# Kernel optimization log

Measured on AMD Instinct MI355X. Metric: run time of the kernel, lower is better.

Reference implementation:

```python
import jax, jax.numpy as jnp
import numpy as np

NUM_HEADS = 8      # in_channels // num_head_channels = 512 // 64
NUM_GROUPS = 32    # GroupNorm groups
EPS = 1e-5


def setup_inputs() -> dict:
    key = jax.random.key(0)
    ks = jax.random.split(key, 6)
    C = 512
    x = jax.random.normal(ks[0], (8, C, 32, 32), dtype=jnp.float32)
    gn_w = jax.random.normal(ks[1], (C,), dtype=jnp.float32) * 0.1 + 1.0
    gn_b = jax.random.normal(ks[2], (C,), dtype=jnp.float32) * 0.1
    qkv_w = jax.random.normal(ks[3], (3 * C, C), dtype=jnp.float32) / np.sqrt(C)
    qkv_b = jnp.zeros((3 * C,), dtype=jnp.float32)
    # NOTE: original zero-initializes to_out; we use small random weights so the
    # attention path contributes to the output (math is identical).
    out_w = jax.random.normal(ks[4], (C, C), dtype=jnp.float32) * 0.02
    out_b = jax.random.normal(ks[5], (C,), dtype=jnp.float32) * 0.02
    return {"x": x, "gn_w": gn_w, "gn_b": gn_b, "qkv_w": qkv_w,
            "qkv_b": qkv_b, "out_w": out_w, "out_b": out_b}


def _group_norm(net, gn_w, gn_b):
    b, c, t = net.shape
    g = net.reshape(b, NUM_GROUPS, c // NUM_GROUPS, t)
    mu = jnp.mean(g, axis=(2, 3), keepdims=True)
    var = jnp.var(g, axis=(2, 3), keepdims=True)
    n = ((g - mu) * jax.lax.rsqrt(var + EPS)).reshape(b, c, t)
    return n * gn_w[None, :, None] + gn_b[None, :, None]


def reference(x, gn_w, gn_b, qkv_w, qkv_b, out_w, out_b):
    b, c, h, w = x.shape
    area = h * w
    inp = x.reshape(b, c, area)                      # [b, c, t]
    n = _group_norm(inp, gn_w, gn_b)
    # 1x1 conv1d == channel GEMM
    qkv = jnp.einsum('oc,bct->bot', qkv_w, n) + qkv_b[None, :, None]  # [b, 3c, t]
    hd = c // NUM_HEADS
    # split_qkv_after_heads: view(b*H, 3*hd, area) then split along channel
    qkv = qkv.reshape(b * NUM_HEADS, 3 * hd, area)
    q, k, v = qkv[:, :hd], qkv[:, hd:2 * hd], qkv[:, 2 * hd:]
    scale = 1.0 / np.sqrt(np.sqrt(hd))               # sqrt-sqrt per-tensor scale
    attn = jnp.einsum('bct,bcs->bts', q * scale, k * scale)  # [bH, t, s]
    prob = jax.nn.softmax(attn, axis=-1)
    net = jnp.einsum('bts,bcs->bct', prob, v).reshape(b, c, area)
    out = jnp.einsum('oc,bct->bot', out_w, net) + out_b[None, :, None]
    return (inp + out).reshape(b, c, h, w)
```

## Files before the change

### kernel.cpp

```cpp
#include <hip/hip_runtime.h>
#include <hip/hip_bf16.h>

typedef __bf16 bf16_t;
typedef __bf16 bf16x8 __attribute__((ext_vector_type(8)));
typedef __bf16 bf16x4 __attribute__((ext_vector_type(4)));
typedef short  s16x4  __attribute__((ext_vector_type(4)));
typedef float  f32x4  __attribute__((ext_vector_type(4)));

#define B_DIM 8
#define C_DIM 512
#define T_DIM 1024
#define NH 8
#define HD 64

__device__ __forceinline__ f32x4 mfma16_bf16(bf16x4 a, bf16x4 b, f32x4 c) {
    return __builtin_amdgcn_mfma_f32_16x16x16bf16_1k(
        __builtin_bit_cast(s16x4, a), __builtin_bit_cast(s16x4, b), c, 0, 0, 0);
}

__global__ __launch_bounds__(256) void prep_w(const float* __restrict__ w1,
                                              const float* __restrict__ w2,
                                              bf16_t* __restrict__ o1,
                                              bf16_t* __restrict__ o2)
{
    int tid = blockIdx.x * 256 + threadIdx.x;
    for (int p = 0; p < 4; ++p) {
        int q = tid + p * 65536;
        const f32x4* src;
        bf16x4* dst;
        int qq;
        if (q < 196608) { src = (const f32x4*)w1; dst = (bf16x4*)o1; qq = q; }
        else            { src = (const f32x4*)w2; dst = (bf16x4*)o2; qq = q - 196608; }
        f32x4 f = src[qq];
        bf16x4 h;
        for (int j = 0; j < 4; ++j) h[j] = (bf16_t)f[j];
        dst[qq] = h;
    }
}

__global__ __launch_bounds__(256) void gn_kernel(const float* __restrict__ x,
                                                 const float* __restrict__ gw,
                                                 const float* __restrict__ gb,
                                                 bf16_t* __restrict__ n_t)
{
    __shared__ bf16_t sX[16384];
    __shared__ float sred[8];
    int tid = threadIdx.x;
    int bb  = blockIdx.x >> 5;
    int g   = blockIdx.x & 31;
    const f32x4* xg4 = reinterpret_cast<const f32x4*>(x + (size_t)(bb * C_DIM + g * 16) * T_DIM);

    float s = 0.f, sq = 0.f;
    for (int i = 0; i < 16; ++i) {
        int v = tid + i * 256;
        f32x4 f = xg4[v];
        bf16x4 h;
        for (int j = 0; j < 4; ++j) {
            s += f[j]; sq += f[j] * f[j];
            h[j] = (bf16_t)f[j];
        }
        *reinterpret_cast<bf16x4*>(sX + v * 4) = h;
    }
    for (int off = 1; off < 64; off <<= 1) {
        s  += __shfl_xor(s, off);
        sq += __shfl_xor(sq, off);
    }
    int wv = tid >> 6;
    if ((tid & 63) == 0) { sred[wv * 2] = s; sred[wv * 2 + 1] = sq; }
    __syncthreads();
    s  = sred[0] + sred[2] + sred[4] + sred[6];
    sq = sred[1] + sred[3] + sred[5] + sred[7];
    float mean = s * (1.f / 16384.f);
    float var  = sq * (1.f / 16384.f) - mean * mean;
    float rs   = rsqrtf(var + 1e-5f);

    int hf = tid & 1;
    float aa[8], bbias[8];
    for (int j = 0; j < 8; ++j) {
        int c = hf * 8 + j;
        float av = gw[g * 16 + c] * rs;
        aa[j] = av;
        bbias[j] = gb[g * 16 + c] - mean * av;
    }
    bf16_t* ob = n_t + (size_t)bb * T_DIM * C_DIM + g * 16 + hf * 8;
    for (int p = 0; p < 8; ++p) {
        int t = (tid >> 1) + p * 128;
        bf16x8 o;
        for (int j = 0; j < 8; ++j) {
            float xv = (float)sX[(hf * 8 + j) * 1024 + t];
            o[j] = (bf16_t)(xv * aa[j] + bbias[j]);
        }
        *reinterpret_cast<bf16x8*>(ob + (size_t)t * C_DIM) = o;
    }
}

__global__ __launch_bounds__(256) void qkv_gemm_kernel(
    const bf16_t* __restrict__ wqb, const float* __restrict__ bq,
    const bf16_t* __restrict__ n_t, bf16_t* __restrict__ qkv)
{
    __shared__ bf16_t sA[64 * 72];
    __shared__ bf16_t sB[128 * 72];
    int tid = threadIdx.x;
    int w = tid >> 6, lane = tid & 63, quad = lane >> 4, l15 = lane & 15;
    int bx = blockIdx.x;
    int t0 = blockIdx.y * 128;
    int bb = blockIdx.z;
    int o0 = bx * 64;
    const bf16_t* Ab = wqb + (size_t)o0 * C_DIM;
    const bf16_t* Bb = n_t + ((size_t)bb * T_DIM + t0) * C_DIM;

    f32x4 acc[2][4];
    for (int mt = 0; mt < 2; ++mt)
        for (int nt = 0; nt < 4; ++nt)
            acc[mt][nt] = f32x4{0.f, 0.f, 0.f, 0.f};
    int mw0 = (w >> 1) * 32;
    int nw0 = (w & 1) * 64;

    for (int k0 = 0; k0 < C_DIM; k0 += 64) {
        for (int i = 0; i < 2; ++i) {
            int v = tid + i * 256;
            int row = v >> 3, c8 = v & 7;
            *reinterpret_cast<bf16x8*>(sA + row * 72 + c8 * 8) =
                *reinterpret_cast<const bf16x8*>(Ab + (size_t)row * C_DIM + k0 + c8 * 8);
        }
        for (int i = 0; i < 4; ++i) {
            int v = tid + i * 256;
            int row = v >> 3, c8 = v & 7;
            *reinterpret_cast<bf16x8*>(sB + row * 72 + c8 * 8) =
                *reinterpret_cast<const bf16x8*>(Bb + (size_t)row * C_DIM + k0 + c8 * 8);
        }
        __syncthreads();
        for (int kk = 0; kk < 2; ++kk) {
            bf16x8 af[2], bfr[4];
            for (int mt = 0; mt < 2; ++mt)
                af[mt] = *reinterpret_cast<const bf16x8*>(sA + (mw0 + mt * 16 + l15) * 72 + kk * 32 + quad * 8);
            for (int nt = 0; nt < 4; ++nt)
                bfr[nt] = *reinterpret_cast<const bf16x8*>(sB + (nw0 + nt * 16 + l15) * 72 + kk * 32 + quad * 8);
            for (int mt = 0; mt < 2; ++mt)
                for (int nt = 0; nt < 4; ++nt)
                    acc[mt][nt] = __builtin_amdgcn_mfma_f32_16x16x32_bf16(af[mt], bfr[nt], acc[mt][nt], 0, 0, 0);
        }
        __syncthreads();
    }

    int h = bx / 3, type = bx % 3;
    size_t base = ((size_t)(bb * NH + h) * 3 + type) * (64 * 1024);

    if (type < 2) {
        for (int mt = 0; mt < 2; ++mt)
            for (int nt = 0; nt < 4; ++nt)
                for (int r = 0; r < 4; ++r) {
                    int mw = mw0 + mt * 16 + quad * 4 + r;
                    int tl = nw0 + nt * 16 + l15;
                    float v = acc[mt][nt][r] + bq[o0 + mw];
                    sB[tl * 72 + mw] = (bf16_t)v;
                }
        __syncthreads();
        for (int i = 0; i < 4; ++i) {
            int v = tid + i * 256;
            int tl = v >> 3, c8 = v & 7;
            bf16x8 d = *reinterpret_cast<const bf16x8*>(sB + tl * 72 + c8 * 8);
            *reinterpret_cast<bf16x8*>(qkv + base + (size_t)(t0 + tl) * 64 + c8 * 8) = d;
        }
    } else {
        for (int mt = 0; mt < 2; ++mt)
            for (int nt = 0; nt < 4; ++nt)
                for (int r = 0; r < 4; ++r) {
                    int mw = mw0 + mt * 16 + quad * 4 + r;
                    int tl = nw0 + nt * 16 + l15;
                    float v = acc[mt][nt][r] + bq[o0 + mw];
                    sB[mw * 136 + tl] = (bf16_t)v;
                }
        __syncthreads();
        for (int i = 0; i < 4; ++i) {
            int v = tid + i * 256;
            int cc = v >> 4, t8 = (v & 15) * 8;
            bf16x8 d = *reinterpret_cast<const bf16x8*>(sB + cc * 136 + t8);
            *reinterpret_cast<bf16x8*>(qkv + base + (size_t)cc * 1024 + t0 + t8) = d;
        }
    }
}

__global__ __launch_bounds__(256, 6) void attn_kernel(const bf16_t* __restrict__ qkv,
                                                      bf16_t* __restrict__ net_t)
{
    __shared__ bf16_t sK[64 * 72];
    __shared__ bf16_t sV[64 * 72];
    int tid = threadIdx.x;
    int w = tid >> 6, lane = tid & 63, quad = lane >> 4, l15 = lane & 15;
    int bh = blockIdx.x;
    int qt = blockIdx.y;
    size_t qb = (size_t)bh * 3 * 65536;
    const bf16_t* Qg = qkv + qb + (size_t)qt * 4096;
    const bf16_t* Kg = qkv + qb + 65536;
    const bf16_t* Vg = qkv + qb + 2 * 65536;
    const float K2 = 0.125f * 1.44269504088896f;

    bf16x8 qf[2];
    for (int kk = 0; kk < 2; ++kk)
        qf[kk] = *reinterpret_cast<const bf16x8*>(Qg + (size_t)(w * 16 + l15) * 64 + kk * 32 + quad * 8);

    bf16x8 kreg[2], vreg[2];
    for (int i = 0; i < 2; ++i) {
        int v = tid + i * 256;
        kreg[i] = *reinterpret_cast<const bf16x8*>(Kg + (size_t)(v >> 3) * 64 + (v & 7) * 8);
        vreg[i] = *reinterpret_cast<const bf16x8*>(Vg + (size_t)(v >> 3) * 1024 + (v & 7) * 8);
    }

    f32x4 O[4];
    for (int i = 0; i < 4; ++i) O[i] = f32x4{0.f, 0.f, 0.f, 0.f};
    float lsum = 0.f;

    for (int st = 0; st < 16; ++st) {
        __syncthreads();
        for (int i = 0; i < 2; ++i) {
            int v = tid + i * 256;
            *reinterpret_cast<bf16x8*>(sK + (v >> 3) * 72 + (v & 7) * 8) = kreg[i];
            *reinterpret_cast<bf16x8*>(sV + (v >> 3) * 72 + (v & 7) * 8) = vreg[i];
        }
        __syncthreads();
        if (st < 15) {
            int s0n = (st + 1) * 64;
            for (int i = 0; i < 2; ++i) {
                int v = tid + i * 256;
                kreg[i] = *reinterpret_cast<const bf16x8*>(Kg + (size_t)(s0n + (v >> 3)) * 64 + (v & 7) * 8);
                vreg[i] = *reinterpret_cast<const bf16x8*>(Vg + (size_t)(v >> 3) * 1024 + s0n + (v & 7) * 8);
            }
        }

        for (int mt = 0; mt < 4; ++mt) {
            f32x4 S = f32x4{0.f, 0.f, 0.f, 0.f};
            for (int kk = 0; kk < 2; ++kk) {
                bf16x8 kf = *reinterpret_cast<const bf16x8*>(sK + (mt * 16 + l15) * 72 + kk * 32 + quad * 8);
                S = __builtin_amdgcn_mfma_f32_16x16x32_bf16(kf, qf[kk], S, 0, 0, 0);
            }
            bf16x4 pf;
            for (int r = 0; r < 4; ++r) {
                float p = exp2f(S[r] * K2);
                lsum += p;
                pf[r] = (bf16_t)p;
            }
            for (int ct = 0; ct < 4; ++ct) {
                bf16x4 vf = *reinterpret_cast<const bf16x4*>(sV + (ct * 16 + l15) * 72 + mt * 16 + quad * 4);
                O[ct] = mfma16_bf16(vf, pf, O[ct]);
            }
        }
    }

    lsum += __shfl_xor(lsum, 16);
    lsum += __shfl_xor(lsum, 32);
    float inv = 1.f / lsum;

    int bb = bh >> 3, h = bh & 7;
    int t = qt * 64 + w * 16 + l15;
    bf16_t* orow = net_t + ((size_t)bb * T_DIM + t) * C_DIM + h * 64;
    for (int ct = 0; ct < 4; ++ct) {
        bf16x4 o4;
        for (int r = 0; r < 4; ++r) o4[r] = (bf16_t)(O[ct][r] * inv);
        *reinterpret_cast<bf16x4*>(orow + ct * 16 + quad * 4) = o4;
    }
}

__global__ __launch_bounds__(256) void out_gemm_kernel(
    const bf16_t* __restrict__ wob, const float* __restrict__ bo,
    const bf16_t* __restrict__ net_t, const float* __restrict__ x,
    float* __restrict__ out)
{
    __shared__ bf16_t sA[64 * 72];
    __shared__ bf16_t sB[128 * 72];
    int tid = threadIdx.x;
    int w = tid >> 6, lane = tid & 63, quad = lane >> 4, l15 = lane & 15;
    int o0 = blockIdx.x * 64;
    int t0 = blockIdx.y * 128;
    int bb = blockIdx.z;
    const bf16_t* Ab = wob + (size_t)o0 * C_DIM;
    const bf16_t* Bb = net_t + ((size_t)bb * T_DIM + t0) * C_DIM;

    f32x4 acc[2][4];
    for (int mt = 0; mt < 2; ++mt)
        for (int nt = 0; nt < 4; ++nt)
            acc[mt][nt] = f32x4{0.f, 0.f, 0.f, 0.f};
    int mw0 = (w >> 1) * 32;
    int nw0 = (w & 1) * 64;

    for (int k0 = 0; k0 < C_DIM; k0 += 64) {
        for (int i = 0; i < 2; ++i) {
            int v = tid + i * 256;
            int row = v >> 3, c8 = v & 7;
            *reinterpret_cast<bf16x8*>(sA + row * 72 + c8 * 8) =
                *reinterpret_cast<const bf16x8*>(Ab + (size_t)row * C_DIM + k0 + c8 * 8);
        }
        for (int i = 0; i < 4; ++i) {
            int v = tid + i * 256;
            int row = v >> 3, c8 = v & 7;
            *reinterpret_cast<bf16x8*>(sB + row * 72 + c8 * 8) =
                *reinterpret_cast<const bf16x8*>(Bb + (size_t)row * C_DIM + k0 + c8 * 8);
        }
        __syncthreads();
        for (int kk = 0; kk < 2; ++kk) {
            bf16x8 af[2], bfr[4];
            for (int mt = 0; mt < 2; ++mt)
                af[mt] = *reinterpret_cast<const bf16x8*>(sA + (mw0 + mt * 16 + l15) * 72 + kk * 32 + quad * 8);
            for (int nt = 0; nt < 4; ++nt)
                bfr[nt] = *reinterpret_cast<const bf16x8*>(sB + (nw0 + nt * 16 + l15) * 72 + kk * 32 + quad * 8);
            for (int mt = 0; mt < 2; ++mt)
                for (int nt = 0; nt < 4; ++nt)
                    acc[mt][nt] = __builtin_amdgcn_mfma_f32_16x16x32_bf16(af[mt], bfr[nt], acc[mt][nt], 0, 0, 0);
        }
        __syncthreads();
    }

    for (int mt = 0; mt < 2; ++mt)
        for (int nt = 0; nt < 4; ++nt)
            for (int r = 0; r < 4; ++r) {
                int o = o0 + mw0 + mt * 16 + quad * 4 + r;
                int t = t0 + nw0 + nt * 16 + l15;
                size_t idx = ((size_t)bb * C_DIM + o) * T_DIM + t;
                out[idx] = acc[mt][nt][r] + bo[o] + x[idx];
            }
}

extern "C" void kernel_launch(void* const* d_in, const int* in_sizes, int n_in,
                              void* d_out, int out_size, void* d_ws, size_t ws_size,
                              hipStream_t stream)
{
    const float* x     = (const float*)d_in[0];
    const float* gn_w  = (const float*)d_in[1];
    const float* gn_b  = (const float*)d_in[2];
    const float* qkv_w = (const float*)d_in[3];
    const float* qkv_b = (const float*)d_in[4];
    const float* out_w = (const float*)d_in[5];
    const float* out_b = (const float*)d_in[6];
    float* out = (float*)d_out;

    char* ws = (char*)d_ws;
    bf16_t* n_t   = (bf16_t*)(ws);
    bf16_t* qkv   = (bf16_t*)(ws + 8388608);
    bf16_t* net_t = (bf16_t*)(ws + 33554432);
    bf16_t* wqb   = (bf16_t*)(ws + 41943040);
    bf16_t* wob   = (bf16_t*)(ws + 41943040 + 1572864);

    prep_w<<<dim3(256), 256, 0, stream>>>(qkv_w, out_w, wqb, wob);
    gn_kernel<<<dim3(256), 256, 0, stream>>>(x, gn_w, gn_b, n_t);
    qkv_gemm_kernel<<<dim3(24, 8, 8), 256, 0, stream>>>(wqb, qkv_b, n_t, qkv);
    attn_kernel<<<dim3(64, 16), 256, 0, stream>>>(qkv, net_t);
    out_gemm_kernel<<<dim3(8, 8, 8), 256, 0, stream>>>(wob, out_b, net_t, x, out);
}
```

Before: 162.5 us.

## Split attention KV tiles across warps and reduce partial outputs through shared memory

```diff
diff --git a/kernel.cpp b/kernel.cpp
--- a/kernel.cpp
+++ b/kernel.cpp
@@ -181,11 +181,15 @@
     }
 }
 
-__global__ __launch_bounds__(256, 6) void attn_kernel(const bf16_t* __restrict__ qkv,
-                                                      bf16_t* __restrict__ net_t)
-{
-    __shared__ bf16_t sK[64 * 72];
-    __shared__ bf16_t sV[64 * 72];
+__global__ __launch_bounds__(256) void attn_kernel(const bf16_t* __restrict__ qkv,
+                                                   bf16_t* __restrict__ net_t)
+{
+    __shared__ __align__(16) char smem[37888];
+    bf16_t* sK = (bf16_t*)smem;
+    bf16_t* sV = (bf16_t*)(smem + 9216);
+    bf16_t* sO = (bf16_t*)smem;
+    float*  sL = (float*)(smem + 36864);
+
     int tid = threadIdx.x;
     int w = tid >> 6, lane = tid & 63, quad = lane >> 4, l15 = lane & 15;
     int bh = blockIdx.x;
@@ -196,9 +200,11 @@
     const bf16_t* Vg = qkv + qb + 2 * 65536;
     const float K2 = 0.125f * 1.44269504088896f;
 
-    bf16x8 qf[2];
-    for (int kk = 0; kk < 2; ++kk)
-        qf[kk] = *reinterpret_cast<const bf16x8*>(Qg + (size_t)(w * 16 + l15) * 64 + kk * 32 + quad * 8);
+    bf16x8 qf[4][2];
+    for (int nt = 0; nt < 4; ++nt)
+        for (int kk = 0; kk < 2; ++kk)
+            qf[nt][kk] = *reinterpret_cast<const bf16x8*>(
+                Qg + (size_t)(nt * 16 + l15) * 64 + kk * 32 + quad * 8);
 
     bf16x8 kreg[2], vreg[2];
     for (int i = 0; i < 2; ++i) {
@@ -207,9 +213,11 @@
         vreg[i] = *reinterpret_cast<const bf16x8*>(Vg + (size_t)(v >> 3) * 1024 + (v & 7) * 8);
     }
 
-    f32x4 O[4];
-    for (int i = 0; i < 4; ++i) O[i] = f32x4{0.f, 0.f, 0.f, 0.f};
-    float lsum = 0.f;
+    f32x4 O[4][4];
+    for (int ct = 0; ct < 4; ++ct)
+        for (int nt = 0; nt < 4; ++nt)
+            O[ct][nt] = f32x4{0.f, 0.f, 0.f, 0.f};
+    float lsum[4] = {0.f, 0.f, 0.f, 0.f};
 
     for (int st = 0; st < 16; ++st) {
         __syncthreads();
@@ -228,37 +236,67 @@
             }
         }
 
-        for (int mt = 0; mt < 4; ++mt) {
-            f32x4 S = f32x4{0.f, 0.f, 0.f, 0.f};
-            for (int kk = 0; kk < 2; ++kk) {
-                bf16x8 kf = *reinterpret_cast<const bf16x8*>(sK + (mt * 16 + l15) * 72 + kk * 32 + quad * 8);
-                S = __builtin_amdgcn_mfma_f32_16x16x32_bf16(kf, qf[kk], S, 0, 0, 0);
+        f32x4 S[4];
+        for (int nt = 0; nt < 4; ++nt) S[nt] = f32x4{0.f, 0.f, 0.f, 0.f};
+        for (int kk = 0; kk < 2; ++kk) {
+            bf16x8 kf = *reinterpret_cast<const bf16x8*>(sK + (w * 16 + l15) * 72 + kk * 32 + quad * 8);
+            for (int nt = 0; nt < 4; ++nt)
+                S[nt] = __builtin_amdgcn_mfma_f32_16x16x32_bf16(kf, qf[nt][kk], S[nt], 0, 0, 0);
+        }
+
+        bf16x4 pf[4];
+        for (int nt = 0; nt < 4; ++nt)
+            for (int r = 0; r < 4; ++r) {
+                float p = exp2f(S[nt][r] * K2);
+                lsum[nt] += p;
+                pf[nt][r] = (bf16_t)p;
             }
-            bf16x4 pf;
-            for (int r = 0; r < 4; ++r) {
-                float p = exp2f(S[r] * K2);
-                lsum += p;
-                pf[r] = (bf16_t)p;
-            }
-            for (int ct = 0; ct < 4; ++ct) {
-                bf16x4 vf = *reinterpret_cast<const bf16x4*>(sV + (ct * 16 + l15) * 72 + mt * 16 + quad * 4);
-                O[ct] = mfma16_bf16(vf, pf, O[ct]);
-            }
-        }
-    }
-
-    lsum += __shfl_xor(lsum, 16);
-    lsum += __shfl_xor(lsum, 32);
-    float inv = 1.f / lsum;
-
+
+        for (int ct = 0; ct < 4; ++ct) {
+            bf16x4 vf = *reinterpret_cast<const bf16x4*>(sV + (ct * 16 + l15) * 72 + w * 16 + quad * 4);
+            for (int nt = 0; nt < 4; ++nt)
+                O[ct][nt] = mfma16_bf16(vf, pf[nt], O[ct][nt]);
+        }
+    }
+
+    for (int nt = 0; nt < 4; ++nt) {
+        lsum[nt] += __shfl_xor(lsum[nt], 16);
+        lsum[nt] += __shfl_xor(lsum[nt], 32);
+    }
+
+    __syncthreads();
+    if (quad == 0)
+        for (int nt = 0; nt < 4; ++nt)
+            sL[w * 64 + nt * 16 + l15] = lsum[nt];
+    for (int ct = 0; ct < 4; ++ct)
+        for (int nt = 0; nt < 4; ++nt) {
+            bf16x4 o4;
+            for (int r = 0; r < 4; ++r) o4[r] = (bf16_t)O[ct][nt][r];
+            *reinterpret_cast<bf16x4*>(
+                sO + ((size_t)w * 64 + nt * 16 + l15) * 72 + ct * 16 + quad * 4) = o4;
+        }
+    __syncthreads();
+
+    int q = tid >> 2, ch = tid & 3;
+    float linv = 1.f / (sL[q] + sL[64 + q] + sL[128 + q] + sL[192 + q]);
+    float acc[16];
+    for (int e = 0; e < 16; ++e) acc[e] = 0.f;
+    for (int ww = 0; ww < 4; ++ww) {
+        const bf16_t* src = sO + ((size_t)ww * 64 + q) * 72 + ch * 16;
+        bf16x8 a = *reinterpret_cast<const bf16x8*>(src);
+        bf16x8 b = *reinterpret_cast<const bf16x8*>(src + 8);
+        for (int e = 0; e < 8; ++e) { acc[e] += (float)a[e]; acc[8 + e] += (float)b[e]; }
+    }
     int bb = bh >> 3, h = bh & 7;
-    int t = qt * 64 + w * 16 + l15;
-    bf16_t* orow = net_t + ((size_t)bb * T_DIM + t) * C_DIM + h * 64;
-    for (int ct = 0; ct < 4; ++ct) {
-        bf16x4 o4;
-        for (int r = 0; r < 4; ++r) o4[r] = (bf16_t)(O[ct][r] * inv);
-        *reinterpret_cast<bf16x4*>(orow + ct * 16 + quad * 4) = o4;
-    }
+    int t = qt * 64 + q;
+    bf16_t* orow = net_t + ((size_t)bb * T_DIM + t) * C_DIM + h * 64 + ch * 16;
+    bf16x8 o1, o2;
+    for (int e = 0; e < 8; ++e) {
+        o1[e] = (bf16_t)(acc[e] * linv);
+        o2[e] = (bf16_t)(acc[8 + e] * linv);
+    }
+    *reinterpret_cast<bf16x8*>(orow) = o1;
+    *reinterpret_cast<bf16x8*>(orow + 8) = o2;
 }
 
 __global__ __launch_bounds__(256) void out_gemm_kernel(
```

Result: slower. 170.2 us (+4.7%).

## Split GroupNorm into stats and apply passes, merge weight conversion into stats

Applied to the files above, without the earlier changes.

```diff
diff --git a/kernel.cpp b/kernel.cpp
--- a/kernel.cpp
+++ b/kernel.cpp
@@ -18,48 +18,41 @@
         __builtin_bit_cast(s16x4, a), __builtin_bit_cast(s16x4, b), c, 0, 0, 0);
 }
 
-__global__ __launch_bounds__(256) void prep_w(const float* __restrict__ w1,
-                                              const float* __restrict__ w2,
-                                              bf16_t* __restrict__ o1,
-                                              bf16_t* __restrict__ o2)
-{
-    int tid = blockIdx.x * 256 + threadIdx.x;
-    for (int p = 0; p < 4; ++p) {
-        int q = tid + p * 65536;
-        const f32x4* src;
-        bf16x4* dst;
-        int qq;
-        if (q < 196608) { src = (const f32x4*)w1; dst = (bf16x4*)o1; qq = q; }
-        else            { src = (const f32x4*)w2; dst = (bf16x4*)o2; qq = q - 196608; }
-        f32x4 f = src[qq];
-        bf16x4 h;
-        for (int j = 0; j < 4; ++j) h[j] = (bf16_t)f[j];
-        dst[qq] = h;
-    }
-}
-
-__global__ __launch_bounds__(256) void gn_kernel(const float* __restrict__ x,
-                                                 const float* __restrict__ gw,
-                                                 const float* __restrict__ gb,
-                                                 bf16_t* __restrict__ n_t)
-{
-    __shared__ bf16_t sX[16384];
+__global__ __launch_bounds__(256) void gn_stats_prep(const float* __restrict__ x,
+                                                     const float* __restrict__ w1,
+                                                     const float* __restrict__ w2,
+                                                     float* __restrict__ stats,
+                                                     bf16_t* __restrict__ o1,
+                                                     bf16_t* __restrict__ o2)
+{
+    int tid = threadIdx.x;
+    int bx = blockIdx.x;
+    if (bx >= 256) {
+        int gt = (bx - 256) * 256 + tid;
+        for (int p = 0; p < 4; ++p) {
+            int q = gt + p * 65536;
+            const f32x4* src;
+            bf16x4* dst;
+            int qq;
+            if (q < 196608) { src = (const f32x4*)w1; dst = (bf16x4*)o1; qq = q; }
+            else            { src = (const f32x4*)w2; dst = (bf16x4*)o2; qq = q - 196608; }
+            f32x4 f = src[qq];
+            bf16x4 h;
+            for (int j = 0; j < 4; ++j) h[j] = (bf16_t)f[j];
+            dst[qq] = h;
+        }
+        return;
+    }
+
     __shared__ float sred[8];
-    int tid = threadIdx.x;
-    int bb  = blockIdx.x >> 5;
-    int g   = blockIdx.x & 31;
+    int bb = bx >> 5;
+    int g  = bx & 31;
     const f32x4* xg4 = reinterpret_cast<const f32x4*>(x + (size_t)(bb * C_DIM + g * 16) * T_DIM);
 
     float s = 0.f, sq = 0.f;
     for (int i = 0; i < 16; ++i) {
-        int v = tid + i * 256;
-        f32x4 f = xg4[v];
-        bf16x4 h;
-        for (int j = 0; j < 4; ++j) {
-            s += f[j]; sq += f[j] * f[j];
-            h[j] = (bf16_t)f[j];
-        }
-        *reinterpret_cast<bf16x4*>(sX + v * 4) = h;
+        f32x4 f = xg4[tid + i * 256];
+        for (int j = 0; j < 4; ++j) { s += f[j]; sq += f[j] * f[j]; }
     }
     for (int off = 1; off < 64; off <<= 1) {
         s  += __shfl_xor(s, off);
@@ -68,29 +61,56 @@
     int wv = tid >> 6;
     if ((tid & 63) == 0) { sred[wv * 2] = s; sred[wv * 2 + 1] = sq; }
     __syncthreads();
-    s  = sred[0] + sred[2] + sred[4] + sred[6];
-    sq = sred[1] + sred[3] + sred[5] + sred[7];
-    float mean = s * (1.f / 16384.f);
-    float var  = sq * (1.f / 16384.f) - mean * mean;
-    float rs   = rsqrtf(var + 1e-5f);
-
-    int hf = tid & 1;
-    float aa[8], bbias[8];
-    for (int j = 0; j < 8; ++j) {
-        int c = hf * 8 + j;
-        float av = gw[g * 16 + c] * rs;
-        aa[j] = av;
-        bbias[j] = gb[g * 16 + c] - mean * av;
-    }
-    bf16_t* ob = n_t + (size_t)bb * T_DIM * C_DIM + g * 16 + hf * 8;
-    for (int p = 0; p < 8; ++p) {
-        int t = (tid >> 1) + p * 128;
-        bf16x8 o;
-        for (int j = 0; j < 8; ++j) {
-            float xv = (float)sX[(hf * 8 + j) * 1024 + t];
-            o[j] = (bf16_t)(xv * aa[j] + bbias[j]);
-        }
-        *reinterpret_cast<bf16x8*>(ob + (size_t)t * C_DIM) = o;
+    if (tid == 0) {
+        s  = sred[0] + sred[2] + sred[4] + sred[6];
+        sq = sred[1] + sred[3] + sred[5] + sred[7];
+        float mean = s * (1.f / 16384.f);
+        float var  = sq * (1.f / 16384.f) - mean * mean;
+        stats[(bb * 32 + g) * 2]     = mean;
+        stats[(bb * 32 + g) * 2 + 1] = rsqrtf(var + 1e-5f);
+    }
+}
+
+__global__ __launch_bounds__(256) void gn_apply(const float* __restrict__ x,
+                                                const float* __restrict__ gw,
+                                                const float* __restrict__ gb,
+                                                const float* __restrict__ stats,
+                                                bf16_t* __restrict__ n_t)
+{
+    __shared__ bf16_t sY[32 * 536];
+    __shared__ float aArr[512], bArr[512];
+    int tid = threadIdx.x;
+    int t0 = blockIdx.x * 32;
+    int bb = blockIdx.y;
+
+    for (int i = 0; i < 2; ++i) {
+        int c = tid + i * 256;
+        int g = c >> 4;
+        float mean = stats[(bb * 32 + g) * 2];
+        float rs   = stats[(bb * 32 + g) * 2 + 1];
+        float a = gw[c] * rs;
+        aArr[c] = a;
+        bArr[c] = gb[c] - mean * a;
+    }
+    __syncthreads();
+
+    for (int i = 0; i < 16; ++i) {
+        int v = tid + i * 256;
+        int c = v >> 3, tq = v & 7;
+        f32x4 f = *reinterpret_cast<const f32x4*>(
+            x + ((size_t)(bb * C_DIM + c) * T_DIM + t0 + tq * 4));
+        float a = aArr[c], b = bArr[c];
+        for (int j = 0; j < 4; ++j)
+            sY[(tq * 4 + j) * 536 + c] = (bf16_t)(f[j] * a + b);
+    }
+    __syncthreads();
+
+    for (int i = 0; i < 8; ++i) {
+        int v = tid + i * 256;
+        int t = v >> 6, c8 = v & 63;
+        bf16x8 d = *reinterpret_cast<const bf16x8*>(sY + t * 536 + c8 * 8);
+        *reinterpret_cast<bf16x8*>(
+            n_t + ((size_t)bb * T_DIM + t0 + t) * C_DIM + c8 * 8) = d;
     }
 }
 
@@ -339,9 +359,10 @@
     bf16_t* net_t = (bf16_t*)(ws + 33554432);
     bf16_t* wqb   = (bf16_t*)(ws + 41943040);
     bf16_t* wob   = (bf16_t*)(ws + 41943040 + 1572864);
-
-    prep_w<<<dim3(256), 256, 0, stream>>>(qkv_w, out_w, wqb, wob);
-    gn_kernel<<<dim3(256), 256, 0, stream>>>(x, gn_w, gn_b, n_t);
+    float*  stats = (float*)(ws + 41943040 + 1572864 + 524288);
+
+    gn_stats_prep<<<dim3(512), 256, 0, stream>>>(x, qkv_w, out_w, stats, wqb, wob);
+    gn_apply<<<dim3(32, 8), 256, 0, stream>>>(x, gn_w, gn_b, stats, n_t);
     qkv_gemm_kernel<<<dim3(24, 8, 8), 256, 0, stream>>>(wqb, qkv_b, n_t, qkv);
     attn_kernel<<<dim3(64, 16), 256, 0, stream>>>(qkv, net_t);
     out_gemm_kernel<<<dim3(8, 8, 8), 256, 0, stream>>>(wob, out_b, net_t, x, out);
```

New measurement: 163.4 us. About the same (+0.6%).
